# Performance work log

Measured on AMD Instinct MI355X. Metric: run time of the kernel, lower is better.

## Reference

```python
import jax, jax.numpy as jnp
import numpy as np

M, N, WIDTH, DEPTH = 32768, 4096, 128, 4
KSCALE = 0.02  # keep kernel@act in tanh's active range


def setup_inputs() -> dict:
    key = jax.random.key(0)
    ks = jax.random.split(key, 6)
    act = jax.random.normal(ks[0], (M, WIDTH), dtype=jnp.float32)
    self_act = jax.random.normal(ks[1], (N, WIDTH), dtype=jnp.float32)
    kernel = jax.random.normal(ks[2], (M, N), dtype=jnp.float32) * KSCALE
    self_kernel = jax.random.normal(ks[3], (N, N), dtype=jnp.float32) * KSCALE
    # per-depth params from hk.layer_stack: glorot-uniform weights, zero bias
    limit = np.sqrt(6.0 / (WIDTH + WIDTH))
    weights = jax.random.uniform(ks[4], (DEPTH, WIDTH, WIDTH), dtype=jnp.float32,
                                 minval=-limit, maxval=limit)
    bias = jnp.zeros((DEPTH, WIDTH), dtype=jnp.float32)
    return {"act": act, "self_act": self_act, "kernel": kernel,
            "self_kernel": self_kernel, "weights": weights, "bias": bias}


def reference(act, self_act, kernel, self_kernel, weights, bias):
    # One depth step (shared W,b used for both branches, as in ScatteringLayer
    # instantiated once per scattering_fn):
    #   act      += tanh((kernel @ self_act) @ W.T + b)        [M, width]
    #   self_act += tanh((self_kernel @ self_act) @ W.T + b)   [N, width]
    # (deterministic=True -> dropout is a no-op; safe_key=None requires it)
    def step(carry, params):
        a, s = carry
        W, b = params
        msg = jnp.einsum('mn,nk->mk', kernel, s)        # kernel message pass
        self_msg = jnp.einsum('nm,mk->nk', self_kernel, s)
        a = a + jnp.tanh(jnp.einsum('mk,ik->mi', msg, W) + b)
        s = s + jnp.tanh(jnp.einsum('nk,ik->ni', self_msg, W) + b)
        return (a, s), None

    (act_out, self_act_out), _ = jax.lax.scan(step, (act, self_act), (weights, bias))
    return act_out, self_act_out
```

## Files before the change

kernel.cpp:

```cpp
#include <hip/hip_runtime.h>

#define M_SZ 32768
#define N_SZ 4096
#define DEPTHS 4
#define SPLITK 8
#define KCH 512

typedef __attribute__((ext_vector_type(8))) short bh8;
typedef __attribute__((ext_vector_type(4))) float f4;
typedef unsigned short u16;
typedef unsigned int u32;

#define SBAR() __builtin_amdgcn_s_barrier()
#define FENCE() asm volatile("" ::: "memory")
#define WAITV(n) asm volatile("s_waitcnt vmcnt(" #n ")" ::: "memory")
#define WAITVL(n) asm volatile("s_waitcnt vmcnt(" #n ") lgkmcnt(0)" ::: "memory")

__device__ __forceinline__ u16 f2bf(float f) {
  u32 u = __float_as_uint(f);
  u = (u + 0x7FFFu + ((u >> 16) & 1u)) >> 16;
  return (u16)u;
}

__device__ __forceinline__ float fast_tanh(float x) {
  float ax = __builtin_fabsf(x);
  float e = __builtin_exp2f(ax * 2.8853900817779268f);
  float r = 1.0f - 2.0f * __builtin_amdgcn_rcpf(e + 1.0f);
  return __builtin_copysignf(r, x);
}

__device__ __forceinline__ void async16(const void* g, void* l) {
  __builtin_amdgcn_global_load_lds((const __attribute__((address_space(1))) u32*)g,
                                   (__attribute__((address_space(3))) u32*)l, 16, 0, 0);
}

__global__ void k1_kernel(const float* __restrict__ s, const float* __restrict__ Wd,
                          u16* __restrict__ Ytd) {
  const int n = blockIdx.x * 256 + threadIdx.x;
  const int i0 = blockIdx.y * 8;
  float acc[8] = {0.f, 0.f, 0.f, 0.f, 0.f, 0.f, 0.f, 0.f};
  const float4* srow = (const float4*)(s + (size_t)n * 128);
#pragma unroll 4
  for (int k4 = 0; k4 < 32; ++k4) {
    float4 sv = srow[k4];
#pragma unroll
    for (int ii = 0; ii < 8; ++ii) {
      const float* w = Wd + (i0 + ii) * 128 + k4 * 4;
      acc[ii] = fmaf(sv.x, w[0], acc[ii]);
      acc[ii] = fmaf(sv.y, w[1], acc[ii]);
      acc[ii] = fmaf(sv.z, w[2], acc[ii]);
      acc[ii] = fmaf(sv.w, w[3], acc[ii]);
    }
  }
#pragma unroll
  for (int ii = 0; ii < 8; ++ii)
    Ytd[(size_t)(i0 + ii) * 4096 + n] = f2bf(acc[ii]);
}

__global__ __launch_bounds__(512, 4) void k2a_kernel(
    const float* __restrict__ SK, const u16* __restrict__ Ytd, float* __restrict__ Zp) {
  __shared__ char smem[8192 + 2 * 16384];
  char* sA = smem;
  char* sB0 = smem + 8192;
  char* sB1 = smem + 8192 + 16384;
  const int t = threadIdx.x, lane = t & 63, wid = t >> 6;
  const int nb = blockIdx.x, c = blockIdx.y;
  const int n0 = nb * 64;
  const int kbz = c * KCH;
  const int wr = wid >> 1, wc = wid & 1;
  const int l15 = lane & 15, l4 = lane >> 4;

  const int arow = t >> 3, kseg8 = t & 7;
  const float4* agz = (const float4*)(SK + (size_t)(n0 + arow) * 4096 + kbz + kseg8 * 8);
  const int awoff = arow * 128 + ((kseg8 ^ (arow & 7)) << 4);

  int bcol[2], bgq[2], bldst[2];
#pragma unroll
  for (int j = 0; j < 2; ++j) {
    int G = j * 512 + t;
    bcol[j] = G >> 3;
    bgq[j] = (G & 7) ^ (bcol[j] & 7);
    bldst[j] = G * 16;
  }

  int aro, bro[4];
  {
    int row = wr * 16 + l15;
    aro = row * 128 + ((l4 ^ (row & 7)) << 4);
  }
#pragma unroll
  for (int n2 = 0; n2 < 4; ++n2) {
    int col = wc * 64 + n2 * 16 + l15;
    bro[n2] = col * 128 + ((l4 ^ (col & 7)) << 4);
  }

  f4 acc[4];
#pragma unroll
  for (int j = 0; j < 4; ++j) acc[j] = (f4){0.f, 0.f, 0.f, 0.f};

  float4 va0 = agz[0], va1 = agz[1];
  FENCE();
  async16(Ytd + (size_t)bcol[0] * 4096 + kbz + bgq[0] * 8, sB0 + bldst[0]);
  async16(Ytd + (size_t)bcol[1] * 4096 + kbz + bgq[1] * 8, sB0 + bldst[1]);
  FENCE();
  char* sBc = sB0;
  char* sBn = sB1;
  for (int k = 0; k < 7; ++k) {
    SBAR(); FENCE();
    WAITV(2);
    union { bh8 v; u16 u[8]; } p;
    p.u[0] = f2bf(va0.x); p.u[1] = f2bf(va0.y); p.u[2] = f2bf(va0.z); p.u[3] = f2bf(va0.w);
    p.u[4] = f2bf(va1.x); p.u[5] = f2bf(va1.y); p.u[6] = f2bf(va1.z); p.u[7] = f2bf(va1.w);
    *(bh8*)(sA + awoff) = p.v;
    FENCE();
    va0 = agz[(k + 1) * 16]; va1 = agz[(k + 1) * 16 + 1];
    FENCE();
    WAITVL(2);
    SBAR(); FENCE();
    async16(Ytd + (size_t)bcol[0] * 4096 + kbz + bgq[0] * 8 + (k + 1) * 64, sBn + bldst[0]);
    async16(Ytd + (size_t)bcol[1] * 4096 + kbz + bgq[1] * 8 + (k + 1) * 64, sBn + bldst[1]);
    FENCE();
#pragma unroll
    for (int kk = 0; kk < 2; ++kk) {
      bh8 a = *(const bh8*)(sA + (aro ^ (kk << 6)));
#pragma unroll
      for (int n2 = 0; n2 < 4; ++n2) {
        bh8 bb = *(const bh8*)(sBc + (bro[n2] ^ (kk << 6)));
        acc[n2] = __builtin_amdgcn_mfma_f32_16x16x32_bf16(a, bb, acc[n2], 0, 0, 0);
      }
    }
    char* tp = sBc; sBc = sBn; sBn = tp;
  }
  SBAR(); FENCE();
  WAITV(2);
  {
    union { bh8 v; u16 u[8]; } p;
    p.u[0] = f2bf(va0.x); p.u[1] = f2bf(va0.y); p.u[2] = f2bf(va0.z); p.u[3] = f2bf(va0.w);
    p.u[4] = f2bf(va1.x); p.u[5] = f2bf(va1.y); p.u[6] = f2bf(va1.z); p.u[7] = f2bf(va1.w);
    *(bh8*)(sA + awoff) = p.v;
  }
  WAITVL(0);
  SBAR(); FENCE();
#pragma unroll
  for (int kk = 0; kk < 2; ++kk) {
    bh8 a = *(const bh8*)(sA + (aro ^ (kk << 6)));
#pragma unroll
    for (int n2 = 0; n2 < 4; ++n2) {
      bh8 bb = *(const bh8*)(sBc + (bro[n2] ^ (kk << 6)));
      acc[n2] = __builtin_amdgcn_mfma_f32_16x16x32_bf16(a, bb, acc[n2], 0, 0, 0);
    }
  }

  float* Z = Zp + (size_t)c * (N_SZ * 128) + (size_t)n0 * 128;
#pragma unroll
  for (int n2 = 0; n2 < 4; ++n2)
#pragma unroll
    for (int q = 0; q < 4; ++q) {
      int r = wr * 16 + l4 * 4 + q;
      int cc = wc * 64 + n2 * 16 + l15;
      Z[r * 128 + cc] = acc[n2][q];
    }
}

__global__ void k2b_kernel(const float* __restrict__ s_src, float* __restrict__ s_dst,
                           const float* __restrict__ Zp, const float* __restrict__ bd) {
  int idx = blockIdx.x * 256 + threadIdx.x;
  float v = bd[idx & 127];
#pragma unroll
  for (int c = 0; c < SPLITK; ++c) v += Zp[(size_t)c * (N_SZ * 128) + idx];
  s_dst[idx] = s_src[idx] + fast_tanh(v);
}

__global__ __launch_bounds__(256, 2) void kb1_kernel(
    const float* __restrict__ s_src, float* __restrict__ s_dst,
    const float* __restrict__ Zp, const float* __restrict__ bd,
    const float* __restrict__ Wnext, u16* __restrict__ Ytnext) {
  __shared__ float sS[16 * 132];
  __shared__ float wlds[128 * 131];
  const int t = threadIdx.x;
  const int n0 = blockIdx.x * 16;

#pragma unroll 8
  for (int j = 0; j < 64; ++j) {
    int li = j * 256 + t;
    int wr_ = li >> 7, wc_ = li & 127;
    wlds[wr_ * 131 + wc_] = Wnext[wr_ * 128 + wc_];
  }

#pragma unroll
  for (int e = 0; e < 8; ++e) {
    int idx = e * 256 + t;
    int r = idx >> 7, c = idx & 127;
    size_t gi = (size_t)(n0 + r) * 128 + c;
    float v = bd[c];
#pragma unroll
    for (int cc = 0; cc < SPLITK; ++cc) v += Zp[(size_t)cc * (N_SZ * 128) + gi];
    float res = s_src[gi] + fast_tanh(v);
    s_dst[gi] = res;
    sS[r * 132 + c] = res;
  }
  __syncthreads();

  const int i = t & 127, nh = t >> 7;
  float acc[8] = {0.f, 0.f, 0.f, 0.f, 0.f, 0.f, 0.f, 0.f};
  const float* wrow = wlds + i * 131;
#pragma unroll 4
  for (int k4 = 0; k4 < 32; ++k4) {
    float w0 = wrow[k4 * 4 + 0], w1 = wrow[k4 * 4 + 1];
    float w2 = wrow[k4 * 4 + 2], w3 = wrow[k4 * 4 + 3];
#pragma unroll
    for (int r = 0; r < 8; ++r) {
      float4 sv = *(const float4*)(sS + (nh * 8 + r) * 132 + k4 * 4);
      acc[r] = fmaf(sv.x, w0, acc[r]);
      acc[r] = fmaf(sv.y, w1, acc[r]);
      acc[r] = fmaf(sv.z, w2, acc[r]);
      acc[r] = fmaf(sv.w, w3, acc[r]);
    }
  }
  union { bh8 v; u16 u[8]; } o;
#pragma unroll
  for (int r = 0; r < 8; ++r) o.u[r] = f2bf(acc[r]);
  *(bh8*)(Ytnext + (size_t)i * 4096 + n0 + nh * 8) = o.v;
}

__global__ __launch_bounds__(1024, 4) void pB_kernel(
    const float* __restrict__ A, const u16* __restrict__ Yt,
    const float* __restrict__ act, const float* __restrict__ bias,
    float* __restrict__ outA) {
  __shared__ char smem[16384 + 2 * 65536];
  char* sA = smem;
  char* sB0 = smem + 16384;
  char* sB1 = smem + 16384 + 65536;
  const int t = threadIdx.x, lane = t & 63, wid = t >> 6;
  const int wr = wid >> 3, wc = wid & 7;
  const int m0 = blockIdx.x * 128;
  const int l15 = lane & 15, l4 = lane >> 4;

  const int arow = t >> 3, kseg8 = t & 7;
  const float4* agp = (const float4*)(A + (size_t)(m0 + arow) * 4096 + kseg8 * 8);
  const int awoff = arow * 128 + ((kseg8 ^ (arow & 7)) << 4);

  const u16* bsrc[4];
  int bldst[4];
#pragma unroll
  for (int j = 0; j < 4; ++j) {
    int G = j * 1024 + t;
    int col = G >> 3;
    int gq = (G & 7) ^ (col & 7);
    bsrc[j] = Yt + (size_t)col * 4096 + gq * 8;
    bldst[j] = G * 16;
  }

  int aro[4], bro[4];
#pragma unroll
  for (int mf = 0; mf < 4; ++mf) {
    int row = wr * 64 + mf * 16 + l15;
    aro[mf] = row * 128 + ((l4 ^ (row & 7)) << 4);
  }
#pragma unroll
  for (int d = 0; d < 4; ++d) {
    int tc = d * 128 + wc * 16 + l15;
    bro[d] = tc * 128 + ((l4 ^ (tc & 7)) << 4);
  }

  f4 acc[4][4];
#pragma unroll
  for (int i = 0; i < 4; ++i)
#pragma unroll
    for (int j = 0; j < 4; ++j) acc[i][j] = (f4){0.f, 0.f, 0.f, 0.f};

  float4 va0 = agp[0], va1 = agp[1];
  FENCE();
#pragma unroll
  for (int j = 0; j < 4; ++j) async16(bsrc[j], sB0 + bldst[j]);
  FENCE();

  char* sBc = sB0;
  char* sBn = sB1;
#pragma unroll 1
  for (int k = 0; k < 63; ++k) {
    SBAR(); FENCE();
    WAITV(4);
    union { bh8 v; u16 u[8]; } p;
    p.u[0] = f2bf(va0.x); p.u[1] = f2bf(va0.y); p.u[2] = f2bf(va0.z); p.u[3] = f2bf(va0.w);
    p.u[4] = f2bf(va1.x); p.u[5] = f2bf(va1.y); p.u[6] = f2bf(va1.z); p.u[7] = f2bf(va1.w);
    *(bh8*)(sA + awoff) = p.v;
    FENCE();
    va0 = agp[(k + 1) * 16]; va1 = agp[(k + 1) * 16 + 1];
    FENCE();
    WAITVL(2);
    SBAR(); FENCE();
#pragma unroll
    for (int j = 0; j < 4; ++j) async16(bsrc[j] + (k + 1) * 64, sBn + bldst[j]);
    FENCE();
#pragma unroll
    for (int kk = 0; kk < 2; ++kk) {
      bh8 af[4];
#pragma unroll
      for (int mf = 0; mf < 4; ++mf) af[mf] = *(const bh8*)(sA + (aro[mf] ^ (kk << 6)));
#pragma unroll
      for (int d = 0; d < 4; ++d) {
        bh8 b = *(const bh8*)(sBc + (bro[d] ^ (kk << 6)));
#pragma unroll
        for (int mf = 0; mf < 4; ++mf)
          acc[mf][d] = __builtin_amdgcn_mfma_f32_16x16x32_bf16(af[mf], b, acc[mf][d], 0, 0, 0);
      }
    }
    char* tp = sBc; sBc = sBn; sBn = tp;
  }
  SBAR(); FENCE();
  WAITV(4);
  {
    union { bh8 v; u16 u[8]; } p;
    p.u[0] = f2bf(va0.x); p.u[1] = f2bf(va0.y); p.u[2] = f2bf(va0.z); p.u[3] = f2bf(va0.w);
    p.u[4] = f2bf(va1.x); p.u[5] = f2bf(va1.y); p.u[6] = f2bf(va1.z); p.u[7] = f2bf(va1.w);
    *(bh8*)(sA + awoff) = p.v;
  }
  WAITVL(0);
  SBAR(); FENCE();
#pragma unroll
  for (int kk = 0; kk < 2; ++kk) {
    bh8 af[4];
#pragma unroll
    for (int mf = 0; mf < 4; ++mf) af[mf] = *(const bh8*)(sA + (aro[mf] ^ (kk << 6)));
#pragma unroll
    for (int d = 0; d < 4; ++d) {
      bh8 b = *(const bh8*)(sBc + (bro[d] ^ (kk << 6)));
#pragma unroll
      for (int mf = 0; mf < 4; ++mf)
        acc[mf][d] = __builtin_amdgcn_mfma_f32_16x16x32_bf16(af[mf], b, acc[mf][d], 0, 0, 0);
    }
  }

  float bsv[4];
#pragma unroll
  for (int d = 0; d < 4; ++d) bsv[d] = bias[d * 128 + wc * 16 + l15];
#pragma unroll
  for (int mf = 0; mf < 4; ++mf)
#pragma unroll
    for (int q = 0; q < 4; ++q) {
      int r = m0 + wr * 64 + mf * 16 + l4 * 4 + q;
      int c = wc * 16 + l15;
      float s = 0.f;
#pragma unroll
      for (int d = 0; d < 4; ++d) s += fast_tanh(acc[mf][d][q] + bsv[d]);
      size_t o = (size_t)r * 128 + c;
      outA[o] = act[o] + s;
    }
}

extern "C" void kernel_launch(void* const* d_in, const int* in_sizes, int n_in,
                              void* d_out, int out_size, void* d_ws, size_t ws_size,
                              hipStream_t stream) {
  const float* act = (const float*)d_in[0];
  const float* self_act = (const float*)d_in[1];
  const float* kern = (const float*)d_in[2];
  const float* self_kern = (const float*)d_in[3];
  const float* weights = (const float*)d_in[4];
  const float* bias = (const float*)d_in[5];
  float* out = (float*)d_out;
  float* s_buf = out + (size_t)M_SZ * 128;

  char* ws = (char*)d_ws;
  u16* Yt = (u16*)ws;
  float* Zp = (float*)(ws + (4u << 20));

  k1_kernel<<<dim3(16, 16), 256, 0, stream>>>(self_act, weights,
                                              Yt);
  for (int d = 0; d < DEPTHS; ++d) {
    const float* s_src = (d == 0) ? self_act : s_buf;
    k2a_kernel<<<dim3(64, SPLITK), 512, 0, stream>>>(self_kern,
                                                     Yt + (size_t)d * 128 * 4096, Zp);
    if (d < DEPTHS - 1) {
      kb1_kernel<<<256, 256, 0, stream>>>(s_src, s_buf, Zp, bias + d * 128,
                                          weights + (d + 1) * 16384,
                                          Yt + (size_t)(d + 1) * 128 * 4096);
    } else {
      k2b_kernel<<<2048, 256, 0, stream>>>(s_src, s_buf, Zp, bias + d * 128);
    }
  }
  pB_kernel<<<256, 1024, 0, stream>>>(kern, Yt, act, bias, out);
}
```

Measured before the change: 333.9 us.

## Pre-convert self_kernel to bf16 once and async-load both operands in k2a

```diff
diff --git a/kernel.cpp b/kernel.cpp
--- a/kernel.cpp
+++ b/kernel.cpp
@@ -35,8 +35,10 @@
 }
 
 __global__ void k1_kernel(const float* __restrict__ s, const float* __restrict__ Wd,
-                          u16* __restrict__ Ytd) {
-  const int n = blockIdx.x * 256 + threadIdx.x;
+                          u16* __restrict__ Ytd, const float* __restrict__ SK,
+                          u16* __restrict__ SKb) {
+  const int t = threadIdx.x;
+  const int n = blockIdx.x * 256 + t;
   const int i0 = blockIdx.y * 8;
   float acc[8] = {0.f, 0.f, 0.f, 0.f, 0.f, 0.f, 0.f, 0.f};
   const float4* srow = (const float4*)(s + (size_t)n * 128);
@@ -55,14 +57,25 @@
 #pragma unroll
   for (int ii = 0; ii < 8; ++ii)
     Ytd[(size_t)(i0 + ii) * 4096 + n] = f2bf(acc[ii]);
+
+  const size_t cbase = ((size_t)blockIdx.y * 16 + blockIdx.x) * 65536;
+#pragma unroll 4
+  for (int cc = 0; cc < 32; ++cc) {
+    size_t off = cbase + (size_t)cc * 2048 + (size_t)t * 8;
+    float4 u0 = *(const float4*)(SK + off);
+    float4 u1 = *(const float4*)(SK + off + 4);
+    union { bh8 v; u16 u[8]; } pk;
+    pk.u[0] = f2bf(u0.x); pk.u[1] = f2bf(u0.y); pk.u[2] = f2bf(u0.z); pk.u[3] = f2bf(u0.w);
+    pk.u[4] = f2bf(u1.x); pk.u[5] = f2bf(u1.y); pk.u[6] = f2bf(u1.z); pk.u[7] = f2bf(u1.w);
+    *(bh8*)(SKb + off) = pk.v;
+  }
 }
 
 __global__ __launch_bounds__(512, 4) void k2a_kernel(
-    const float* __restrict__ SK, const u16* __restrict__ Ytd, float* __restrict__ Zp) {
-  __shared__ char smem[8192 + 2 * 16384];
-  char* sA = smem;
-  char* sB0 = smem + 8192;
-  char* sB1 = smem + 8192 + 16384;
+    const u16* __restrict__ SKb, const u16* __restrict__ Ytd, float* __restrict__ Zp) {
+  __shared__ char smem[2 * 8192 + 2 * 16384];
+#define SA_BUF(BUF) (smem + (BUF) * 8192)
+#define SB_BUF(BUF) (smem + 16384 + (BUF) * 16384)
   const int t = threadIdx.x, lane = t & 63, wid = t >> 6;
   const int nb = blockIdx.x, c = blockIdx.y;
   const int n0 = nb * 64;
@@ -70,17 +83,25 @@
   const int wr = wid >> 1, wc = wid & 1;
   const int l15 = lane & 15, l4 = lane >> 4;
 
-  const int arow = t >> 3, kseg8 = t & 7;
-  const float4* agz = (const float4*)(SK + (size_t)(n0 + arow) * 4096 + kbz + kseg8 * 8);
-  const int awoff = arow * 128 + ((kseg8 ^ (arow & 7)) << 4);
-
-  int bcol[2], bgq[2], bldst[2];
-#pragma unroll
-  for (int j = 0; j < 2; ++j) {
-    int G = j * 512 + t;
-    bcol[j] = G >> 3;
-    bgq[j] = (G & 7) ^ (bcol[j] & 7);
-    bldst[j] = G * 16;
+  const int arow_g = t >> 3, aseg = t & 7;
+  const int agq = aseg ^ (arow_g & 7);
+  const u16* asrc = SKb + (size_t)(n0 + arow_g) * 4096 + kbz + agq * 8;
+  const int aldst = t * 16;
+
+  const u16* bsrc0;
+  const u16* bsrc1;
+  int bldst0, bldst1;
+  {
+    int G = t;
+    int bcol = G >> 3;
+    int bgq = (G & 7) ^ (bcol & 7);
+    bsrc0 = Ytd + (size_t)bcol * 4096 + kbz + bgq * 8;
+    bldst0 = G * 16;
+    G = 512 + t;
+    bcol = G >> 3;
+    bgq = (G & 7) ^ (bcol & 7);
+    bsrc1 = Ytd + (size_t)bcol * 4096 + kbz + bgq * 8;
+    bldst1 = G * 16;
   }
 
   int aro, bro[4];
@@ -98,58 +119,41 @@
 #pragma unroll
   for (int j = 0; j < 4; ++j) acc[j] = (f4){0.f, 0.f, 0.f, 0.f};
 
-  float4 va0 = agz[0], va1 = agz[1];
+#define K2A_ISSUE(KK, BUF)                                     \
+  {                                                            \
+    async16(asrc + (KK) * 64, SA_BUF(BUF) + aldst);            \
+    async16(bsrc0 + (KK) * 64, SB_BUF(BUF) + bldst0);          \
+    async16(bsrc1 + (KK) * 64, SB_BUF(BUF) + bldst1);          \
+  }
+#define K2A_COMPUTE(BUF)                                                          \
+  {                                                                               \
+    _Pragma("unroll") for (int kk = 0; kk < 2; ++kk) {                            \
+      bh8 a = *(const bh8*)(SA_BUF(BUF) + (aro ^ (kk << 6)));                     \
+      _Pragma("unroll") for (int n2 = 0; n2 < 4; ++n2) {                          \
+        bh8 bb = *(const bh8*)(SB_BUF(BUF) + (bro[n2] ^ (kk << 6)));              \
+        acc[n2] = __builtin_amdgcn_mfma_f32_16x16x32_bf16(a, bb, acc[n2], 0, 0, 0); \
+      }                                                                           \
+    }                                                                             \
+  }
+
+  K2A_ISSUE(0, 0)
+  K2A_ISSUE(1, 1)
   FENCE();
-  async16(Ytd + (size_t)bcol[0] * 4096 + kbz + bgq[0] * 8, sB0 + bldst[0]);
-  async16(Ytd + (size_t)bcol[1] * 4096 + kbz + bgq[1] * 8, sB0 + bldst[1]);
-  FENCE();
-  char* sBc = sB0;
-  char* sBn = sB1;
+#pragma unroll 1
   for (int k = 0; k < 7; ++k) {
+    WAITV(3);
     SBAR(); FENCE();
-    WAITV(2);
-    union { bh8 v; u16 u[8]; } p;
-    p.u[0] = f2bf(va0.x); p.u[1] = f2bf(va0.y); p.u[2] = f2bf(va0.z); p.u[3] = f2bf(va0.w);
-    p.u[4] = f2bf(va1.x); p.u[5] = f2bf(va1.y); p.u[6] = f2bf(va1.z); p.u[7] = f2bf(va1.w);
-    *(bh8*)(sA + awoff) = p.v;
-    FENCE();
-    va0 = agz[(k + 1) * 16]; va1 = agz[(k + 1) * 16 + 1];
-    FENCE();
-    WAITVL(2);
+    K2A_COMPUTE(k & 1)
     SBAR(); FENCE();
-    async16(Ytd + (size_t)bcol[0] * 4096 + kbz + bgq[0] * 8 + (k + 1) * 64, sBn + bldst[0]);
-    async16(Ytd + (size_t)bcol[1] * 4096 + kbz + bgq[1] * 8 + (k + 1) * 64, sBn + bldst[1]);
-    FENCE();
-#pragma unroll
-    for (int kk = 0; kk < 2; ++kk) {
-      bh8 a = *(const bh8*)(sA + (aro ^ (kk << 6)));
-#pragma unroll
-      for (int n2 = 0; n2 < 4; ++n2) {
-        bh8 bb = *(const bh8*)(sBc + (bro[n2] ^ (kk << 6)));
-        acc[n2] = __builtin_amdgcn_mfma_f32_16x16x32_bf16(a, bb, acc[n2], 0, 0, 0);
-      }
-    }
-    char* tp = sBc; sBc = sBn; sBn = tp;
-  }
+    if (k < 6) { K2A_ISSUE(k + 2, k & 1) FENCE(); }
+  }
+  WAITV(0);
   SBAR(); FENCE();
-  WAITV(2);
-  {
-    union { bh8 v; u16 u[8]; } p;
-    p.u[0] = f2bf(va0.x); p.u[1] = f2bf(va0.y); p.u[2] = f2bf(va0.z); p.u[3] = f2bf(va0.w);
-    p.u[4] = f2bf(va1.x); p.u[5] = f2bf(va1.y); p.u[6] = f2bf(va1.z); p.u[7] = f2bf(va1.w);
-    *(bh8*)(sA + awoff) = p.v;
-  }
-  WAITVL(0);
-  SBAR(); FENCE();
-#pragma unroll
-  for (int kk = 0; kk < 2; ++kk) {
-    bh8 a = *(const bh8*)(sA + (aro ^ (kk << 6)));
-#pragma unroll
-    for (int n2 = 0; n2 < 4; ++n2) {
-      bh8 bb = *(const bh8*)(sBc + (bro[n2] ^ (kk << 6)));
-      acc[n2] = __builtin_amdgcn_mfma_f32_16x16x32_bf16(a, bb, acc[n2], 0, 0, 0);
-    }
-  }
+  K2A_COMPUTE(1)
+#undef K2A_ISSUE
+#undef K2A_COMPUTE
+#undef SA_BUF
+#undef SB_BUF
 
   float* Z = Zp + (size_t)c * (N_SZ * 128) + (size_t)n0 * 128;
 #pragma unroll
@@ -364,12 +368,12 @@
   char* ws = (char*)d_ws;
   u16* Yt = (u16*)ws;
   float* Zp = (float*)(ws + (4u << 20));
-
-  k1_kernel<<<dim3(16, 16), 256, 0, stream>>>(self_act, weights,
-                                              Yt);
+  u16* SKb = (u16*)(ws + (20u << 20));
+
+  k1_kernel<<<dim3(16, 16), 256, 0, stream>>>(self_act, weights, Yt, self_kern, SKb);
   for (int d = 0; d < DEPTHS; ++d) {
     const float* s_src = (d == 0) ? self_act : s_buf;
-    k2a_kernel<<<dim3(64, SPLITK), 512, 0, stream>>>(self_kern,
+    k2a_kernel<<<dim3(64, SPLITK), 512, 0, stream>>>(SKb,
                                                      Yt + (size_t)d * 128 * 4096, Zp);
     if (d < DEPTHS - 1) {
       kb1_kernel<<<256, 256, 0, stream>>>(s_src, s_buf, Zp, bias + d * 128,
```

After: 312.9 us. -6.3%, faster.
